# Performance work log

Hardware: AMD Instinct MI355X
Metric: run time of the kernel (lower is better)

Reference implementation:

```python
import jax, jax.numpy as jnp
import numpy as np

GLM_HIDDEN = 256
POS_EMB_DIM = 64
LN_EPS = 1e-5


def _pair_indices(seq_len, K):
    # emo index i (row), cau index j (col); keep |j-i| <= K (static mask)
    i = np.repeat(np.arange(seq_len), seq_len)
    j = np.tile(np.arange(seq_len), seq_len)
    rel = j - i
    keep = np.abs(rel) <= K
    return i[keep], j[keep], rel[keep]


def setup_inputs() -> dict:
    key = jax.random.key(0)
    ks = jax.random.split(key, 8)
    B, S, D, P, K = 32, 128, GLM_HIDDEN, POS_EMB_DIM, 8
    doc_sents_h = jax.random.normal(ks[0], (B, S, D), dtype=jnp.float32)
    pos_emb = jax.random.normal(ks[1], (2 * K + 1, P), dtype=jnp.float32) * 0.1
    in_dim = 2 * D + P
    W1 = jax.random.normal(ks[2], (D, in_dim), dtype=jnp.float32) * (1.0 / np.sqrt(in_dim))
    b1 = jnp.zeros((D,), dtype=jnp.float32)
    ln_g = jnp.ones((D,), dtype=jnp.float32)
    ln_b = jnp.zeros((D,), dtype=jnp.float32)
    W2 = jax.random.normal(ks[3], (1, D), dtype=jnp.float32) * (1.0 / np.sqrt(D))
    b2 = jnp.zeros((1,), dtype=jnp.float32)
    return {"doc_sents_h": doc_sents_h, "pos_emb": pos_emb, "W1": W1, "b1": b1,
            "ln_g": ln_g, "ln_b": ln_b, "W2": W2, "b2": b2, "K": K}


def reference(doc_sents_h, pos_emb, W1, b1, ln_g, ln_b, W2, b2, K):
    B, S, D = doc_sents_h.shape
    ii, jj, rel = _pair_indices(S, K)          # static numpy, shape [n_couple]
    # couples = [H_i ; H_j] for in-window pairs (replaces broadcast-concat + masked_select)
    couples = jnp.concatenate([doc_sents_h[:, ii], doc_sents_h[:, jj]], axis=-1)  # [B,n,2D]
    rel_idx = jnp.asarray(rel + K, dtype=jnp.int32)
    rpe = pos_emb[rel_idx]                     # [n, P]
    rf = jnp.asarray(rel, dtype=jnp.float32)
    kernel = jnp.exp(-jnp.square(rf[:, None] - rf[None, :]))  # [n, n]
    rpe = kernel @ rpe                         # [n, P] (same for every batch elem)
    pair = jnp.concatenate(
        [couples, jnp.broadcast_to(rpe[None], (B,) + rpe.shape)], axis=-1)  # [B,n,2D+P]
    h = jnp.einsum('bnf,df->bnd', pair, W1) + b1
    mu = jnp.mean(h, axis=-1, keepdims=True)
    var = jnp.mean(jnp.square(h - mu), axis=-1, keepdims=True)
    h = (h - mu) * jax.lax.rsqrt(var + LN_EPS) * ln_g + ln_b
    h = jax.nn.elu(h)                          # dropout is identity in eval
    scores = (jnp.einsum('bnd,od->bno', h, W2) + b2)[..., 0]  # [B, n]
    emo_cau_pos = jnp.stack([jnp.asarray(ii + 1), jnp.asarray(jj + 1)], axis=1)  # [n, 2]
    return scores, emo_cau_pos
```

## Files before the change

kernel.cpp:

```cpp
#include <hip/hip_runtime.h>
#include <math.h>

constexpr int kB = 32;
constexpr int kS = 128;
constexpr int kD = 256;
constexpr int kK = 8;
constexpr int kNPair = 2104;
constexpr int kInDim = 576;
constexpr int kRS = 264;

typedef __attribute__((ext_vector_type(8))) short short8;
typedef __attribute__((ext_vector_type(4))) float f32x4;
typedef unsigned int u32;

__device__ inline ushort f2b(float f) {
  union { float f; uint u; } v; v.f = f;
  uint r = v.u + 0x7FFF + ((v.u >> 16) & 1);
  return (ushort)(r >> 16);
}

__device__ inline void gload16(const void* g, void* lds) {
  __builtin_amdgcn_global_load_lds(
      (const u32 __attribute__((address_space(1)))*)g,
      (u32 __attribute__((address_space(3)))*)lds, 16, 0, 0);
}

__global__ __launch_bounds__(256) void prep(
    const float* __restrict__ H, const float* __restrict__ pos_emb,
    const float* __restrict__ W1, const float* __restrict__ b1,
    ushort* __restrict__ Hb, ushort* __restrict__ Wb, float* __restrict__ Rg) {
  const int blk = blockIdx.x, tid = threadIdx.x;
  if (blk < 256) {
#pragma unroll
    for (int l = 0; l < 4; ++l) {
      int c = blk * 1024 + l * 256 + tid;
      int row = c >> 6, kq = (c & 63) << 2;
      float4 a = *(const float4*)(H + row * kD + kq);
      ushort4 u; u.x = f2b(a.x); u.y = f2b(a.y); u.z = f2b(a.z); u.w = f2b(a.w);
      *(ushort4*)(Hb + row * 256 + (kq ^ ((row & 7) << 3))) = u;
    }
  } else if (blk < 288) {
    int bb = blk - 256;
#pragma unroll
    for (int l = 0; l < 4; ++l) {
      int c = bb * 1024 + l * 256 + tid;
      int r = c >> 6;
      int kq = (c & 63) << 2;
      int nt = r >> 6, rr = r & 63;
      const float* src = W1 + (r & 255) * kInDim + ((r < 256) ? 0 : 256) + kq;
      float4 a = *(const float4*)src;
      ushort4 u; u.x = f2b(a.x); u.y = f2b(a.y); u.z = f2b(a.z); u.w = f2b(a.w);
      *(ushort4*)(Wb + (nt * 64 + rr) * 256 + (kq ^ ((rr & 7) << 3))) = u;
    }
  } else {
    __shared__ float pe[17 * 64];
    for (int idx = tid; idx < 17 * 64; idx += 256) pe[idx] = pos_emb[idx];
    __syncthreads();
    const int d = tid;
    float w[64];
    const float* wr = W1 + d * kInDim + 512;
#pragma unroll
    for (int q = 0; q < 16; ++q) {
      float4 t4 = *(const float4*)(wr + q * 4);
      w[q * 4 + 0] = t4.x; w[q * 4 + 1] = t4.y;
      w[q * 4 + 2] = t4.z; w[q * 4 + 3] = t4.w;
    }
    float acc[17];
#pragma unroll
    for (int t = 0; t < 17; ++t) acc[t] = 0.f;
    for (int u = 0; u < 17; ++u) {
      float m = 0.f;
#pragma unroll
      for (int p = 0; p < 64; ++p) m += pe[u * 64 + p] * w[p];
      int au = u - kK; if (au < 0) au = -au;
      m *= (float)(kS - au);
#pragma unroll
      for (int t = 0; t < 17; ++t) {
        int dd = t - u;
        acc[t] += expf((float)(-(dd * dd))) * m;
      }
    }
#pragma unroll
    for (int t = 0; t < 17; ++t) Rg[t * kD + d] = acc[t] + b1[d];
  }
}

__global__ __launch_bounds__(512, 2) void fused2(
    const ushort* __restrict__ Hb, const ushort* __restrict__ Wb,
    const float* __restrict__ Rg,
    const float* __restrict__ ln_g, const float* __restrict__ ln_b,
    const float* __restrict__ W2, const float* __restrict__ b2,
    float* __restrict__ out) {
  __shared__ __align__(16) ushort sH[48 * 256];
  __shared__ __align__(16) ushort sW[64 * 256];
  __shared__ float sU[16 * kRS];
  __shared__ float sV[48 * kRS];
  __shared__ float sR[17 * kRS];
  __shared__ float sG[256], sBe[256], sWo[256];

  const int tid = threadIdx.x;
  const int lane = tid & 63;
  const int b = blockIdx.x >> 3;
  const int i0 = (blockIdx.x & 7) << 4;
  int ws_ = i0 - 16; if (ws_ < 0) ws_ = 0; if (ws_ > 80) ws_ = 80;
  const int ws = ws_;
  const int oi = i0 - ws;

  {
    const ushort* src = Hb + (b * kS + ws) * 256;
    for (int idx = tid; idx < 1536; idx += 512)
      gload16(src + idx * 8, (char*)sH + (idx - lane) * 16);
  }
  for (int idx = tid; idx < 2048; idx += 512)
    gload16(Wb + idx * 8, (char*)sW + (idx - lane) * 16);
  if (tid < 256) { sG[tid] = ln_g[tid]; sBe[tid] = ln_b[tid]; sWo[tid] = W2[tid]; }
  for (int idx = tid; idx < 1088; idx += 512) {
    float4 a = *(const float4*)(Rg + idx * 4);
    int t = idx >> 6, d = (idx & 63) << 2;
    *(float4*)&sR[t * kRS + d] = a;
  }
  __syncthreads();

  const int w = tid >> 6;
  const int lr = lane & 15;
  const int lk = (lane >> 4) << 3;
  const int swz = (lr & 7) << 3;
  const int r0 = (lane >> 4) << 2;

  for (int nt = 0; nt < 8; ++nt) {
    f32x4 acc[3] = {{0,0,0,0},{0,0,0,0},{0,0,0,0}};
    if (w < 4) {
      const int brow = (w << 4) + lr;
#pragma unroll
      for (int kk = 0; kk < 8; ++kk) {
        int k0 = (kk << 5) + lk;
        short8 bf = *(const short8*)(const void*)&sW[brow * 256 + (k0 ^ swz)];
#pragma unroll
        for (int m = 0; m < 3; ++m) {
          short8 af = *(const short8*)(const void*)&sH[(m * 16 + lr) * 256 + (k0 ^ swz)];
          acc[m] = __builtin_amdgcn_mfma_f32_16x16x32_bf16(af, bf, acc[m], 0, 0, 0);
        }
      }
    }
    __syncthreads();
    if (nt < 7) {
      const ushort* src = Wb + (nt + 1) * 16384;
      for (int idx = tid; idx < 2048; idx += 512)
        gload16(src + idx * 8, (char*)sW + (idx - lane) * 16);
    }
    if (w < 4) {
      const int cg = (nt << 6) + (w << 4) + lr;
#pragma unroll
      for (int m = 0; m < 3; ++m)
#pragma unroll
        for (int r = 0; r < 4; ++r) {
          int rw = m * 16 + r0 + r;
          float val = acc[m][r];
          if (cg < 256) { unsigned ur = (unsigned)(rw - oi); if (ur < 16u) sU[ur * kRS + cg] = val; }
          else sV[rw * kRS + (cg - 256)] = val;
        }
    }
    __syncthreads();
  }

  const int g = tid >> 4, l16 = tid & 15;
  const int ir = g >> 1;
  const int tbeg = (g & 1) ? 9 : 0;
  const int tend = (g & 1) ? 17 : 9;
  const int i = i0 + ir;

  float ureg[16];
#pragma unroll
  for (int q = 0; q < 4; ++q) {
    float4 u4 = *(const float4*)&sU[ir * kRS + (q << 6) + (l16 << 2)];
    ureg[q * 4 + 0] = u4.x; ureg[q * 4 + 1] = u4.y;
    ureg[q * 4 + 2] = u4.z; ureg[q * 4 + 3] = u4.w;
  }
  float4 Gp[4], Bp[4], Wp[4];
#pragma unroll
  for (int q = 0; q < 4; ++q) {
    int d = (q << 6) + (l16 << 2);
    Gp[q] = *(const float4*)&sG[d];
    Bp[q] = *(const float4*)&sBe[d];
    Wp[q] = *(const float4*)&sWo[d];
  }
  const float bias2 = b2[0];

  int start_i;
  if (i <= 8)        start_i = (i * i + 17 * i) / 2;
  else if (i <= 120) start_i = 100 + (i - 8) * 17;
  else { int m = i - 120; start_i = 2004 + 16 * m - (m * (m - 1)) / 2; }
  const int lower = (i - kK > 0) ? (i - kK) : 0;

  for (int t = tbeg; t < tend; ++t) {
    int j = i - kK + t;
    if (j < 0 || j >= kS) continue;
    const int vr = j - ws;
    const int p = start_i + (j - lower);
    const float* Vr = &sV[vr * kRS];
    const float* Rr = &sR[t * kRS];

    float h[16]; float ssum = 0.f, qsum = 0.f;
#pragma unroll
    for (int q = 0; q < 4; ++q) {
      int d = (q << 6) + (l16 << 2);
      float4 v4 = *(const float4*)(Vr + d);
      float4 r4 = *(const float4*)(Rr + d);
      float h0 = ureg[q * 4 + 0] + v4.x + r4.x;
      float h1 = ureg[q * 4 + 1] + v4.y + r4.y;
      float h2 = ureg[q * 4 + 2] + v4.z + r4.z;
      float h3 = ureg[q * 4 + 3] + v4.w + r4.w;
      h[q * 4 + 0] = h0; h[q * 4 + 1] = h1; h[q * 4 + 2] = h2; h[q * 4 + 3] = h3;
      ssum += h0 + h1 + h2 + h3;
      qsum += h0 * h0 + h1 * h1 + h2 * h2 + h3 * h3;
    }
#pragma unroll
    for (int off = 8; off > 0; off >>= 1) {
      ssum += __shfl_xor(ssum, off);
      qsum += __shfl_xor(qsum, off);
    }
    const float mu = ssum * (1.0f / kD);
    const float var = qsum * (1.0f / kD) - mu * mu;
    const float rs = rsqrtf(var + 1e-5f);
    float dot = 0.f;
#pragma unroll
    for (int q = 0; q < 4; ++q) {
      float y0 = (h[q * 4 + 0] - mu) * rs * Gp[q].x + Bp[q].x;
      float y1 = (h[q * 4 + 1] - mu) * rs * Gp[q].y + Bp[q].y;
      float y2 = (h[q * 4 + 2] - mu) * rs * Gp[q].z + Bp[q].z;
      float y3 = (h[q * 4 + 3] - mu) * rs * Gp[q].w + Bp[q].w;
      y0 = y0 > 0.f ? y0 : (__expf(y0) - 1.0f);
      y1 = y1 > 0.f ? y1 : (__expf(y1) - 1.0f);
      y2 = y2 > 0.f ? y2 : (__expf(y2) - 1.0f);
      y3 = y3 > 0.f ? y3 : (__expf(y3) - 1.0f);
      dot += y0 * Wp[q].x + y1 * Wp[q].y + y2 * Wp[q].z + y3 * Wp[q].w;
    }
#pragma unroll
    for (int off = 8; off > 0; off >>= 1) dot += __shfl_xor(dot, off);

    if (l16 == 0) {
      out[b * kNPair + p] = dot + bias2;
      if (b == 0) {
        float* po = out + kB * kNPair;
        po[2 * p + 0] = (float)(i + 1);
        po[2 * p + 1] = (float)(j + 1);
      }
    }
  }
}

extern "C" void kernel_launch(void* const* d_in, const int* in_sizes, int n_in,
                              void* d_out, int out_size, void* d_ws, size_t ws_size,
                              hipStream_t stream) {
  (void)in_sizes; (void)n_in; (void)ws_size; (void)out_size;
  const float* H       = (const float*)d_in[0];
  const float* pos_emb = (const float*)d_in[1];
  const float* W1      = (const float*)d_in[2];
  const float* b1      = (const float*)d_in[3];
  const float* ln_g    = (const float*)d_in[4];
  const float* ln_b    = (const float*)d_in[5];
  const float* W2      = (const float*)d_in[6];
  const float* b2      = (const float*)d_in[7];
  float* out = (float*)d_out;

  ushort* Hb = (ushort*)d_ws;
  ushort* Wb = Hb + 4096 * 256;
  float*  Rg = (float*)(Wb + 512 * 256);

  prep<<<289, 256, 0, stream>>>(H, pos_emb, W1, b1, Hb, Wb, Rg);
  fused2<<<kB * 8, 512, 0, stream>>>(Hb, Wb, Rg, ln_g, ln_b, W2, b2, out);
}
```

Measured before the change: 46.15 us.

## Fuse prep into single kernel with direct fp32-to-bf16 MFMA operand loads

```diff
diff --git a/kernel.cpp b/kernel.cpp
--- a/kernel.cpp
+++ b/kernel.cpp
@@ -1,4 +1,5 @@
 #include <hip/hip_runtime.h>
+#include <hip/hip_bf16.h>
 #include <math.h>
 
 constexpr int kB = 32;
@@ -7,55 +8,43 @@
 constexpr int kK = 8;
 constexpr int kNPair = 2104;
 constexpr int kInDim = 576;
-constexpr int kRS = 264;
+constexpr int kRS = 260;
 
 typedef __attribute__((ext_vector_type(8))) short short8;
 typedef __attribute__((ext_vector_type(4))) float f32x4;
-typedef unsigned int u32;
-
-__device__ inline ushort f2b(float f) {
-  union { float f; uint u; } v; v.f = f;
-  uint r = v.u + 0x7FFF + ((v.u >> 16) & 1);
-  return (ushort)(r >> 16);
+
+__device__ inline short8 pack8(float4 p, float4 q) {
+  union { short8 s; __hip_bfloat162 h[4]; } u;
+  u.h[0] = __float22bfloat162_rn(make_float2(p.x, p.y));
+  u.h[1] = __float22bfloat162_rn(make_float2(p.z, p.w));
+  u.h[2] = __float22bfloat162_rn(make_float2(q.x, q.y));
+  u.h[3] = __float22bfloat162_rn(make_float2(q.z, q.w));
+  return u.s;
 }
 
-__device__ inline void gload16(const void* g, void* lds) {
-  __builtin_amdgcn_global_load_lds(
-      (const u32 __attribute__((address_space(1)))*)g,
-      (u32 __attribute__((address_space(3)))*)lds, 16, 0, 0);
-}
-
-__global__ __launch_bounds__(256) void prep(
+__global__ __launch_bounds__(1024, 4) void fused(
     const float* __restrict__ H, const float* __restrict__ pos_emb,
     const float* __restrict__ W1, const float* __restrict__ b1,
-    ushort* __restrict__ Hb, ushort* __restrict__ Wb, float* __restrict__ Rg) {
-  const int blk = blockIdx.x, tid = threadIdx.x;
-  if (blk < 256) {
-#pragma unroll
-    for (int l = 0; l < 4; ++l) {
-      int c = blk * 1024 + l * 256 + tid;
-      int row = c >> 6, kq = (c & 63) << 2;
-      float4 a = *(const float4*)(H + row * kD + kq);
-      ushort4 u; u.x = f2b(a.x); u.y = f2b(a.y); u.z = f2b(a.z); u.w = f2b(a.w);
-      *(ushort4*)(Hb + row * 256 + (kq ^ ((row & 7) << 3))) = u;
-    }
-  } else if (blk < 288) {
-    int bb = blk - 256;
-#pragma unroll
-    for (int l = 0; l < 4; ++l) {
-      int c = bb * 1024 + l * 256 + tid;
-      int r = c >> 6;
-      int kq = (c & 63) << 2;
-      int nt = r >> 6, rr = r & 63;
-      const float* src = W1 + (r & 255) * kInDim + ((r < 256) ? 0 : 256) + kq;
-      float4 a = *(const float4*)src;
-      ushort4 u; u.x = f2b(a.x); u.y = f2b(a.y); u.z = f2b(a.z); u.w = f2b(a.w);
-      *(ushort4*)(Wb + (nt * 64 + rr) * 256 + (kq ^ ((rr & 7) << 3))) = u;
-    }
-  } else {
-    __shared__ float pe[17 * 64];
-    for (int idx = tid; idx < 17 * 64; idx += 256) pe[idx] = pos_emb[idx];
-    __syncthreads();
+    const float* __restrict__ ln_g, const float* __restrict__ ln_b,
+    const float* __restrict__ W2, const float* __restrict__ b2,
+    float* __restrict__ out) {
+  __shared__ float sU[16 * kRS];
+  __shared__ float sV[32 * kRS];
+  __shared__ float sR[17 * kRS];
+  __shared__ float sG[256], sBe[256], sWo[256];
+
+  const int tid = threadIdx.x;
+  const int b = blockIdx.x >> 3;
+  const int i0 = (blockIdx.x & 7) << 4;
+  int ws_ = i0 - 8; if (ws_ < 0) ws_ = 0; if (ws_ > 96) ws_ = 96;
+  const int ws = ws_;
+  const int oi = i0 - ws;
+
+  if (tid >= 256 && tid < 512) {
+    int t2 = tid - 256;
+    sG[t2] = ln_g[t2]; sBe[t2] = ln_b[t2]; sWo[t2] = W2[t2];
+  }
+  if (tid < 256) {
     const int d = tid;
     float w[64];
     const float* wr = W1 + d * kInDim + 512;
@@ -65,108 +54,81 @@
       w[q * 4 + 0] = t4.x; w[q * 4 + 1] = t4.y;
       w[q * 4 + 2] = t4.z; w[q * 4 + 3] = t4.w;
     }
-    float acc[17];
-#pragma unroll
-    for (int t = 0; t < 17; ++t) acc[t] = 0.f;
+    float m[17];
+#pragma unroll
     for (int u = 0; u < 17; ++u) {
-      float m = 0.f;
-#pragma unroll
-      for (int p = 0; p < 64; ++p) m += pe[u * 64 + p] * w[p];
+      float s = 0.f;
+#pragma unroll
+      for (int p = 0; p < 16; ++p) {
+        float4 pe = *(const float4*)(pos_emb + u * 64 + p * 4);
+        s += pe.x * w[p * 4] + pe.y * w[p * 4 + 1] + pe.z * w[p * 4 + 2] + pe.w * w[p * 4 + 3];
+      }
       int au = u - kK; if (au < 0) au = -au;
-      m *= (float)(kS - au);
-#pragma unroll
-      for (int t = 0; t < 17; ++t) {
-        int dd = t - u;
-        acc[t] += expf((float)(-(dd * dd))) * m;
-      }
-    }
-#pragma unroll
-    for (int t = 0; t < 17; ++t) Rg[t * kD + d] = acc[t] + b1[d];
-  }
-}
-
-__global__ __launch_bounds__(512, 2) void fused2(
-    const ushort* __restrict__ Hb, const ushort* __restrict__ Wb,
-    const float* __restrict__ Rg,
-    const float* __restrict__ ln_g, const float* __restrict__ ln_b,
-    const float* __restrict__ W2, const float* __restrict__ b2,
-    float* __restrict__ out) {
-  __shared__ __align__(16) ushort sH[48 * 256];
-  __shared__ __align__(16) ushort sW[64 * 256];
-  __shared__ float sU[16 * kRS];
-  __shared__ float sV[48 * kRS];
-  __shared__ float sR[17 * kRS];
-  __shared__ float sG[256], sBe[256], sWo[256];
-
-  const int tid = threadIdx.x;
+      m[u] = s * (float)(kS - au);
+    }
+#pragma unroll
+    for (int t = 0; t < 17; ++t) {
+      float a = 0.f;
+#pragma unroll
+      for (int u = 0; u < 17; ++u) {
+        float e = __expf((float)(-(t - u) * (t - u)));
+        a += e * m[u];
+      }
+      sR[t * kRS + d] = a + b1[d];
+    }
+  }
+
   const int lane = tid & 63;
-  const int b = blockIdx.x >> 3;
-  const int i0 = (blockIdx.x & 7) << 4;
-  int ws_ = i0 - 16; if (ws_ < 0) ws_ = 0; if (ws_ > 80) ws_ = 80;
-  const int ws = ws_;
-  const int oi = i0 - ws;
-
-  {
-    const ushort* src = Hb + (b * kS + ws) * 256;
-    for (int idx = tid; idx < 1536; idx += 512)
-      gload16(src + idx * 8, (char*)sH + (idx - lane) * 16);
-  }
-  for (int idx = tid; idx < 2048; idx += 512)
-    gload16(Wb + idx * 8, (char*)sW + (idx - lane) * 16);
-  if (tid < 256) { sG[tid] = ln_g[tid]; sBe[tid] = ln_b[tid]; sWo[tid] = W2[tid]; }
-  for (int idx = tid; idx < 1088; idx += 512) {
-    float4 a = *(const float4*)(Rg + idx * 4);
-    int t = idx >> 6, d = (idx & 63) << 2;
-    *(float4*)&sR[t * kRS + d] = a;
-  }
-  __syncthreads();
-
-  const int w = tid >> 6;
+  const int wv = tid >> 6;
   const int lr = lane & 15;
   const int lk = (lane >> 4) << 3;
-  const int swz = (lr & 7) << 3;
-  const int r0 = (lane >> 4) << 2;
-
-  for (int nt = 0; nt < 8; ++nt) {
-    f32x4 acc[3] = {{0,0,0,0},{0,0,0,0},{0,0,0,0}};
-    if (w < 4) {
-      const int brow = (w << 4) + lr;
-#pragma unroll
-      for (int kk = 0; kk < 8; ++kk) {
-        int k0 = (kk << 5) + lk;
-        short8 bf = *(const short8*)(const void*)&sW[brow * 256 + (k0 ^ swz)];
-#pragma unroll
-        for (int m = 0; m < 3; ++m) {
-          short8 af = *(const short8*)(const void*)&sH[(m * 16 + lr) * 256 + (k0 ^ swz)];
-          acc[m] = __builtin_amdgcn_mfma_f32_16x16x32_bf16(af, bf, acc[m], 0, 0, 0);
+  const int rt = wv & 1;
+  {
+    const float* Arow = H + (b * kS + ws + rt * 16 + lr) * kD + lk;
+    short8 a[8];
+#pragma unroll
+    for (int kk = 0; kk < 8; ++kk) {
+      float4 p = *(const float4*)(Arow + kk * 32);
+      float4 q = *(const float4*)(Arow + kk * 32 + 4);
+      a[kk] = pack8(p, q);
+    }
+#pragma unroll
+    for (int ci = 0; ci < 4; ++ci) {
+      const int ct = (wv >> 1) * 4 + ci;
+      const int c = ct * 16 + lr;
+      const float* Brow = W1 + (c & 255) * kInDim + ((c < 256) ? 0 : 256) + lk;
+      f32x4 acc0 = {0.f, 0.f, 0.f, 0.f}, acc1 = {0.f, 0.f, 0.f, 0.f};
+#pragma unroll
+      for (int kk = 0; kk < 8; kk += 2) {
+        float4 p0 = *(const float4*)(Brow + kk * 32);
+        float4 q0 = *(const float4*)(Brow + kk * 32 + 4);
+        short8 bf0 = pack8(p0, q0);
+        acc0 = __builtin_amdgcn_mfma_f32_16x16x32_bf16(a[kk], bf0, acc0, 0, 0, 0);
+        float4 p1 = *(const float4*)(Brow + (kk + 1) * 32);
+        float4 q1 = *(const float4*)(Brow + (kk + 1) * 32 + 4);
+        short8 bf1 = pack8(p1, q1);
+        acc1 = __builtin_amdgcn_mfma_f32_16x16x32_bf16(a[kk + 1], bf1, acc1, 0, 0, 0);
+      }
+      const int rb = rt * 16 + ((lane >> 4) << 2);
+#pragma unroll
+      for (int r = 0; r < 4; ++r) {
+        float val = acc0[r] + acc1[r];
+        int wr2 = rb + r;
+        if (c < 256) {
+          unsigned ur = (unsigned)(wr2 - oi);
+          if (ur < 16u) sU[ur * kRS + c] = val;
+        } else {
+          sV[wr2 * kRS + (c - 256)] = val;
         }
       }
     }
-    __syncthreads();
-    if (nt < 7) {
-      const ushort* src = Wb + (nt + 1) * 16384;
-      for (int idx = tid; idx < 2048; idx += 512)
-        gload16(src + idx * 8, (char*)sW + (idx - lane) * 16);
-    }
-    if (w < 4) {
-      const int cg = (nt << 6) + (w << 4) + lr;
-#pragma unroll
-      for (int m = 0; m < 3; ++m)
-#pragma unroll
-        for (int r = 0; r < 4; ++r) {
-          int rw = m * 16 + r0 + r;
-          float val = acc[m][r];
-          if (cg < 256) { unsigned ur = (unsigned)(rw - oi); if (ur < 16u) sU[ur * kRS + cg] = val; }
-          else sV[rw * kRS + (cg - 256)] = val;
-        }
-    }
-    __syncthreads();
-  }
+  }
+  __syncthreads();
 
   const int g = tid >> 4, l16 = tid & 15;
-  const int ir = g >> 1;
-  const int tbeg = (g & 1) ? 9 : 0;
-  const int tend = (g & 1) ? 17 : 9;
+  const int ir = g >> 2, qq = g & 3;
+  const int tb = qq * 4 + (qq > 0);
+  const int te = qq * 4 + 5;
   const int i = i0 + ir;
 
   float ureg[16];
@@ -189,15 +151,14 @@
   int start_i;
   if (i <= 8)        start_i = (i * i + 17 * i) / 2;
   else if (i <= 120) start_i = 100 + (i - 8) * 17;
-  else { int m = i - 120; start_i = 2004 + 16 * m - (m * (m - 1)) / 2; }
+  else { int mm = i - 120; start_i = 2004 + 16 * mm - (mm * (mm - 1)) / 2; }
   const int lower = (i - kK > 0) ? (i - kK) : 0;
 
-  for (int t = tbeg; t < tend; ++t) {
+  for (int t = tb; t < te; ++t) {
     int j = i - kK + t;
     if (j < 0 || j >= kS) continue;
-    const int vr = j - ws;
     const int p = start_i + (j - lower);
-    const float* Vr = &sV[vr * kRS];
+    const float* Vr = &sV[(j - ws) * kRS];
     const float* Rr = &sR[t * kRS];
 
     float h[16]; float ssum = 0.f, qsum = 0.f;
@@ -252,7 +213,7 @@
 extern "C" void kernel_launch(void* const* d_in, const int* in_sizes, int n_in,
                               void* d_out, int out_size, void* d_ws, size_t ws_size,
                               hipStream_t stream) {
-  (void)in_sizes; (void)n_in; (void)ws_size; (void)out_size;
+  (void)in_sizes; (void)n_in; (void)d_ws; (void)ws_size; (void)out_size;
   const float* H       = (const float*)d_in[0];
   const float* pos_emb = (const float*)d_in[1];
   const float* W1      = (const float*)d_in[2];
@@ -263,10 +224,5 @@
   const float* b2      = (const float*)d_in[7];
   float* out = (float*)d_out;
 
-  ushort* Hb = (ushort*)d_ws;
-  ushort* Wb = Hb + 4096 * 256;
-  float*  Rg = (float*)(Wb + 512 * 256);
-
-  prep<<<289, 256, 0, stream>>>(H, pos_emb, W1, b1, Hb, Wb, Rg);
-  fused2<<<kB * 8, 512, 0, stream>>>(Hb, Wb, Rg, ln_g, ln_b, W2, b2, out);
+  fused<<<kB * 8, 1024, 0, stream>>>(H, pos_emb, W1, b1, ln_g, ln_b, W2, b2, out);
 }
```

Measured after the change: 53.29 us. +15.5%, slower.
